# Optimization experiments

Hardware: AMD Instinct MI355X
Metric: run time of the kernel (lower is better)

The kernel has to match this reference:

```python
import jax, jax.numpy as jnp
import numpy as np

TAU_MEM, TAU_SYN = 20.0, 5.0
THRESHOLD, BETA, RESET = 1.0, 4.0, 0.0
ALPHA_MEM = float(np.exp(-1.0 / TAU_MEM))
ALPHA_SYN = float(np.exp(-1.0 / TAU_SYN))
EPS = 1e-6


def _lif(x, W, b):
    # x: [B,T,D] -> spikes_with_grad: [B,T,H] (faithful to original incl. the
    # spikes + stop_grad(spikes - surrogate) expression, forward value 2*s - sg)
    cur = jnp.einsum('btd,dh->bth', x, W) + b  # all-timestep projection (same math as per-step dense)
    B, T, H = cur.shape
    v0 = jnp.zeros((B, H), cur.dtype)
    i0 = jnp.zeros((B, H), cur.dtype)

    def step(carry, ic):
        v, i = carry
        i = ALPHA_SYN * i + ic
        v = ALPHA_MEM * v + (1.0 - ALPHA_MEM) * i
        spikes = (v >= THRESHOLD).astype(jnp.float32)
        sg = BETA / (2.0 * (1.0 + jnp.cosh(BETA * (v - THRESHOLD))))
        swg = spikes + jax.lax.stop_gradient(spikes - sg)
        v = jnp.where(spikes > 0, RESET, v)
        return (v, i), swg

    (_, _), out = jax.lax.scan(step, (v0, i0), cur.transpose(1, 0, 2))
    return out.transpose(1, 0, 2)


def _layernorm(x, scale, bias):
    mu = jnp.mean(x, axis=-1, keepdims=True)
    var = jnp.var(x, axis=-1, keepdims=True)
    return (x - mu) * jax.lax.rsqrt(var + EPS) * scale + bias


def setup_inputs() -> dict:
    key = jax.random.key(0)
    ks = jax.random.split(key, 8)
    B, T, D = 512, 128, 512
    H0, H1, H2, C = 256, 128, 64, 2
    s = 0.02
    return {
        'spike_trains': jax.random.uniform(ks[0], (B, T, D), jnp.float32),
        'W0': jax.random.normal(ks[1], (D, H0), jnp.float32) * s,
        'b0': jnp.zeros((H0,), jnp.float32),
        'ln1_scale': jnp.ones((H0,), jnp.float32),
        'ln1_bias': jnp.zeros((H0,), jnp.float32),
        'W1': jax.random.normal(ks[2], (H0, H1), jnp.float32) * s,
        'b1': jnp.zeros((H1,), jnp.float32),
        'ln2_scale': jnp.ones((H1,), jnp.float32),
        'ln2_bias': jnp.zeros((H1,), jnp.float32),
        'W2': jax.random.normal(ks[3], (H1, H2), jnp.float32) * s,
        'b2': jnp.zeros((H2,), jnp.float32),
        'Wc': jax.random.normal(ks[4], (H2, C), jnp.float32) * s,
        'bc': jnp.zeros((C,), jnp.float32),
    }


def reference(spike_trains, W0, b0, ln1_scale, ln1_bias, W1, b1,
              ln2_scale, ln2_bias, W2, b2, Wc, bc):
    x = _lif(spike_trains, W0, b0)                    # layer 0: no pre-norm
    x = _lif(_layernorm(x, ln1_scale, ln1_bias), W1, b1)
    x = _lif(_layernorm(x, ln2_scale, ln2_bias), W2, b2)
    pooled = jnp.mean(x, axis=1)                      # [B, H2]
    logits = pooled @ Wc + bc                         # [B, C]
    return logits, pooled, jnp.mean(x)
```

## Files before the change

kernel.cpp:

```cpp
#include <hip/hip_runtime.h>
#include <cstddef>

static constexpr float A_MEM  = 0.951229424500714f;
static constexpr float A_SYN  = 0.8187307530779818f;
static constexpr float OM_MEM = 0.04877057549928599f;

__global__ __launch_bounds__(256) void gemm_bias(
    const float* __restrict__ A, const float* __restrict__ W,
    const float* __restrict__ bias, float* __restrict__ C,
    int M, int K, int N)
{
    __shared__ float As[16][64];
    __shared__ float Ws[16][64];
    const int tid = threadIdx.x;
    const int tx = tid & 15;
    const int ty = tid >> 4;
    const int mBase = blockIdx.y * 64;
    const int nBase = blockIdx.x * 64;

    const int arow = tid >> 2;
    const int acol = (tid & 3) << 2;
    const int wrow = tid >> 4;
    const int wcol = (tid & 15) << 2;

    float acc[4][4] = {};
    for (int k0 = 0; k0 < K; k0 += 16) {
        float4 av = *(const float4*)(A + (size_t)(mBase + arow) * K + (k0 + acol));
        float4 wv = *(const float4*)(W + (size_t)(k0 + wrow) * N + (nBase + wcol));
        __syncthreads();
        As[acol + 0][arow] = av.x;
        As[acol + 1][arow] = av.y;
        As[acol + 2][arow] = av.z;
        As[acol + 3][arow] = av.w;
        *(float4*)&Ws[wrow][wcol] = wv;
        __syncthreads();
        #pragma unroll
        for (int kk = 0; kk < 16; ++kk) {
            float4 a = *(const float4*)&As[kk][ty << 2];
            float4 b = *(const float4*)&Ws[kk][tx << 2];
            float ar[4] = {a.x, a.y, a.z, a.w};
            float br[4] = {b.x, b.y, b.z, b.w};
            #pragma unroll
            for (int i2 = 0; i2 < 4; ++i2)
                #pragma unroll
                for (int j = 0; j < 4; ++j)
                    acc[i2][j] += ar[i2] * br[j];
        }
    }
    const int cn = nBase + (tx << 2);
    float4 bv = *(const float4*)(bias + cn);
    float bb[4] = {bv.x, bv.y, bv.z, bv.w};
    #pragma unroll
    for (int i2 = 0; i2 < 4; ++i2) {
        const int cm = mBase + (ty << 2) + i2;
        float4 o;
        o.x = acc[i2][0] + bb[0];
        o.y = acc[i2][1] + bb[1];
        o.z = acc[i2][2] + bb[2];
        o.w = acc[i2][3] + bb[3];
        *(float4*)(C + (size_t)cm * N + cn) = o;
    }
}

template<bool POOL>
__global__ __launch_bounds__(256) void lif_scan(
    const float* __restrict__ cur, float* __restrict__ out,
    float* __restrict__ pooled, int T, int H)
{
    const int idx = blockIdx.x * 256 + threadIdx.x;
    const int b = idx / H;
    const int h = idx - b * H;
    const float* cp = cur + (size_t)b * T * H + h;
    float* op = out ? out + (size_t)b * T * H + h : nullptr;
    float v = 0.f, cin = 0.f, sum = 0.f;
    for (int t = 0; t < T; ++t) {
        float ic = cp[(size_t)t * H];
        cin = A_SYN * cin + ic;
        v = A_MEM * v + OM_MEM * cin;
        float s = (v >= 1.0f) ? 1.0f : 0.0f;
        float xx = 4.0f * (v - 1.0f);
        float ch2 = __expf(xx) + __expf(-xx);
        float sg = 4.0f / (2.0f + ch2);
        float o = 2.0f * s - sg;
        if (POOL) sum += o;
        else op[(size_t)t * H] = o;
        if (s > 0.f) v = 0.0f;
    }
    if (POOL) pooled[idx] = sum * (1.0f / 128.0f);
}

template<int H>
__global__ __launch_bounds__(256) void layernorm_k(
    const float* __restrict__ x, const float* __restrict__ scale,
    const float* __restrict__ bias, float* __restrict__ y)
{
    constexpr int VPL = H / 64;
    const int wave = threadIdx.x >> 6;
    const int lane = threadIdx.x & 63;
    const size_t row = (size_t)blockIdx.x * 4 + wave;
    const float* xp = x + row * H + lane * VPL;
    float vals[VPL];
    #pragma unroll
    for (int j = 0; j < VPL; ++j) vals[j] = xp[j];
    float s = 0.f, ss = 0.f;
    #pragma unroll
    for (int j = 0; j < VPL; ++j) { s += vals[j]; ss += vals[j] * vals[j]; }
    #pragma unroll
    for (int off = 32; off; off >>= 1) {
        s  += __shfl_xor(s, off);
        ss += __shfl_xor(ss, off);
    }
    const float mu  = s * (1.0f / H);
    const float var = ss * (1.0f / H) - mu * mu;
    const float rs  = rsqrtf(var + 1e-6f);
    float* yp = y + row * H + lane * VPL;
    #pragma unroll
    for (int j = 0; j < VPL; ++j)
        yp[j] = (vals[j] - mu) * rs * scale[lane * VPL + j] + bias[lane * VPL + j];
}

__global__ __launch_bounds__(1024) void head_k(
    const float* __restrict__ pooled, const float* __restrict__ Wc,
    const float* __restrict__ bc, float* __restrict__ logits,
    float* __restrict__ meanp)
{
    const int tid = threadIdx.x;
    const int b = tid >> 1, c = tid & 1;
    float accl = 0.f;
    #pragma unroll 8
    for (int k = 0; k < 64; ++k) accl += pooled[b * 64 + k] * Wc[k * 2 + c];
    logits[tid] = accl + bc[c];

    float s = 0.f;
    for (int i2 = tid; i2 < 512 * 64; i2 += 1024) s += pooled[i2];
    #pragma unroll
    for (int off = 32; off; off >>= 1) s += __shfl_xor(s, off);
    __shared__ float red[16];
    const int wave = tid >> 6, lane = tid & 63;
    if (lane == 0) red[wave] = s;
    __syncthreads();
    if (tid == 0) {
        float tot = 0.f;
        #pragma unroll
        for (int w = 0; w < 16; ++w) tot += red[w];
        meanp[0] = tot * (1.0f / 32768.0f);
    }
}

extern "C" void kernel_launch(void* const* d_in, const int* in_sizes, int n_in,
                              void* d_out, int out_size, void* d_ws, size_t ws_size,
                              hipStream_t stream) {
    const float* x    = (const float*)d_in[0];
    const float* W0   = (const float*)d_in[1];
    const float* b0   = (const float*)d_in[2];
    const float* ln1s = (const float*)d_in[3];
    const float* ln1b = (const float*)d_in[4];
    const float* W1   = (const float*)d_in[5];
    const float* b1   = (const float*)d_in[6];
    const float* ln2s = (const float*)d_in[7];
    const float* ln2b = (const float*)d_in[8];
    const float* W2   = (const float*)d_in[9];
    const float* b2   = (const float*)d_in[10];
    const float* Wc   = (const float*)d_in[11];
    const float* bc   = (const float*)d_in[12];

    float* out    = (float*)d_out;
    float* logits = out;
    float* pooled = out + 1024;
    float* meanp  = out + 1024 + 32768;

    const int B = 512, T = 128, M = B * T;
    float* bufA = (float*)d_ws;
    float* bufB = bufA + (size_t)M * 256;

    gemm_bias<<<dim3(256 / 64, M / 64), 256, 0, stream>>>(x, W0, b0, bufA, M, 512, 256);
    lif_scan<false><<<(B * 256) / 256, 256, 0, stream>>>(bufA, bufB, nullptr, T, 256);
    layernorm_k<256><<<M / 4, 256, 0, stream>>>(bufB, ln1s, ln1b, bufA);
    gemm_bias<<<dim3(128 / 64, M / 64), 256, 0, stream>>>(bufA, W1, b1, bufB, M, 256, 128);
    lif_scan<false><<<(B * 128) / 256, 256, 0, stream>>>(bufB, bufA, nullptr, T, 128);
    layernorm_k<128><<<M / 4, 256, 0, stream>>>(bufA, ln2s, ln2b, bufB);
    gemm_bias<<<dim3(64 / 64, M / 64), 256, 0, stream>>>(bufB, W2, b2, bufA, M, 128, 64);
    lif_scan<true><<<(B * 64) / 256, 256, 0, stream>>>(bufA, nullptr, pooled, T, 64);
    head_k<<<1, 1024, 0, stream>>>(pooled, Wc, bc, logits, meanp);
}
```

Before: 657.9 us.

## Fuse GEMM, LIF scan and layernorm into one per-batch kernel per layer

Each layer becomes a single kernel with one block per batch element. The block computes the full [128 x H] projection tile in registers, stages it in LDS, runs the LIF scan over time from shared memory, then applies layernorm and writes the next layer's input. This removes the global round-trips of the intermediate currents and spikes and cuts the launch count. The cost is large dynamic shared memory (up to 128 KB), which allows only one block per CU, plus a serial scan that uses only H threads while the others sit idle.

```diff
diff --git a/kernel.cpp b/kernel.cpp
--- a/kernel.cpp
+++ b/kernel.cpp
@@ -5,118 +5,161 @@
 static constexpr float A_SYN  = 0.8187307530779818f;
 static constexpr float OM_MEM = 0.04877057549928599f;
 
-__global__ __launch_bounds__(256) void gemm_bias(
+template<int NT, int K, int H, bool LN, bool POOL>
+__global__ __launch_bounds__(NT) void layer_fused(
     const float* __restrict__ A, const float* __restrict__ W,
-    const float* __restrict__ bias, float* __restrict__ C,
-    int M, int K, int N)
+    const float* __restrict__ bias,
+    const float* __restrict__ lns, const float* __restrict__ lnb,
+    float* __restrict__ out)
 {
-    __shared__ float As[16][64];
-    __shared__ float Ws[16][64];
-    const int tid = threadIdx.x;
-    const int tx = tid & 15;
-    const int ty = tid >> 4;
-    const int mBase = blockIdx.y * 64;
-    const int nBase = blockIdx.x * 64;
-
-    const int arow = tid >> 2;
-    const int acol = (tid & 3) << 2;
-    const int wrow = tid >> 4;
-    const int wcol = (tid & 15) << 2;
-
-    float acc[4][4] = {};
-    for (int k0 = 0; k0 < K; k0 += 16) {
-        float4 av = *(const float4*)(A + (size_t)(mBase + arow) * K + (k0 + acol));
-        float4 wv = *(const float4*)(W + (size_t)(k0 + wrow) * N + (nBase + wcol));
-        __syncthreads();
-        As[acol + 0][arow] = av.x;
-        As[acol + 1][arow] = av.y;
-        As[acol + 2][arow] = av.z;
-        As[acol + 3][arow] = av.w;
-        *(float4*)&Ws[wrow][wcol] = wv;
-        __syncthreads();
+  constexpr int T = 128;
+  constexpr int BK = 16;
+  constexpr int TXB = (NT == 512) ? 5 : 4;
+  constexpr int NTX = 1 << TXB;
+  constexpr int NJ  = H / NTX;
+  constexpr int S   = K / BK;
+  constexpr int APT = (BK * 128 / 4) / NT;
+  constexpr int WPT = (BK * H / 4) / NT < 1 ? 1 : (BK * H / 4) / NT;
+  extern __shared__ __align__(16) float smem[];
+  float* As  = smem;
+  float* Ws  = smem + BK * 128;
+  float* buf = smem;
+
+  const int b   = blockIdx.x;
+  const int tid = threadIdx.x;
+  const int tx  = tid & (NTX - 1);
+  const int ty  = tid >> TXB;
+  const float* Ab = A + (size_t)b * T * K;
+
+  float acc[8][NJ];
+  #pragma unroll
+  for (int i = 0; i < 8; ++i)
+    #pragma unroll
+    for (int j = 0; j < NJ; ++j) acc[i][j] = 0.f;
+
+  float4 aR[APT], wR[WPT];
+  auto load_tile = [&](int k0) {
+    #pragma unroll
+    for (int p = 0; p < APT; ++p) {
+      int f4 = tid + p * NT;
+      int r  = f4 >> 2;
+      int c4 = (f4 & 3) << 2;
+      aR[p] = *(const float4*)(Ab + (size_t)r * K + k0 + c4);
+    }
+    #pragma unroll
+    for (int p = 0; p < WPT; ++p) {
+      int f4 = tid + p * NT;
+      int k  = f4 / (H / 4);
+      int c4 = (f4 % (H / 4)) << 2;
+      wR[p] = *(const float4*)(W + (size_t)(k0 + k) * H + c4);
+    }
+  };
+
+  load_tile(0);
+  for (int s = 0; s < S; ++s) {
+    __syncthreads();
+    #pragma unroll
+    for (int p = 0; p < APT; ++p) {
+      int f4 = tid + p * NT;
+      int r  = f4 >> 2;
+      int c4 = (f4 & 3) << 2;
+      As[(c4 + 0) * 128 + r] = aR[p].x;
+      As[(c4 + 1) * 128 + r] = aR[p].y;
+      As[(c4 + 2) * 128 + r] = aR[p].z;
+      As[(c4 + 3) * 128 + r] = aR[p].w;
+    }
+    #pragma unroll
+    for (int p = 0; p < WPT; ++p) {
+      int f4 = tid + p * NT;
+      int k  = f4 / (H / 4);
+      int c4 = (f4 % (H / 4)) << 2;
+      *(float4*)(Ws + k * H + c4) = wR[p];
+    }
+    __syncthreads();
+    if (s + 1 < S) load_tile((s + 1) * BK);
+    #pragma unroll
+    for (int kk = 0; kk < BK; ++kk) {
+      float4 a0 = *(const float4*)(As + kk * 128 + ty * 8);
+      float4 a1 = *(const float4*)(As + kk * 128 + ty * 8 + 4);
+      float av[8] = {a0.x, a0.y, a0.z, a0.w, a1.x, a1.y, a1.z, a1.w};
+      float bv[NJ];
+      #pragma unroll
+      for (int j = 0; j < NJ; ++j) bv[j] = Ws[kk * H + j * NTX + tx];
+      #pragma unroll
+      for (int i = 0; i < 8; ++i)
         #pragma unroll
-        for (int kk = 0; kk < 16; ++kk) {
-            float4 a = *(const float4*)&As[kk][ty << 2];
-            float4 b = *(const float4*)&Ws[kk][tx << 2];
-            float ar[4] = {a.x, a.y, a.z, a.w};
-            float br[4] = {b.x, b.y, b.z, b.w};
-            #pragma unroll
-            for (int i2 = 0; i2 < 4; ++i2)
-                #pragma unroll
-                for (int j = 0; j < 4; ++j)
-                    acc[i2][j] += ar[i2] * br[j];
-        }
-    }
-    const int cn = nBase + (tx << 2);
-    float4 bv = *(const float4*)(bias + cn);
-    float bb[4] = {bv.x, bv.y, bv.z, bv.w};
-    #pragma unroll
-    for (int i2 = 0; i2 < 4; ++i2) {
-        const int cm = mBase + (ty << 2) + i2;
-        float4 o;
-        o.x = acc[i2][0] + bb[0];
-        o.y = acc[i2][1] + bb[1];
-        o.z = acc[i2][2] + bb[2];
-        o.w = acc[i2][3] + bb[3];
-        *(float4*)(C + (size_t)cm * N + cn) = o;
-    }
-}
-
-template<bool POOL>
-__global__ __launch_bounds__(256) void lif_scan(
-    const float* __restrict__ cur, float* __restrict__ out,
-    float* __restrict__ pooled, int T, int H)
-{
-    const int idx = blockIdx.x * 256 + threadIdx.x;
-    const int b = idx / H;
-    const int h = idx - b * H;
-    const float* cp = cur + (size_t)b * T * H + h;
-    float* op = out ? out + (size_t)b * T * H + h : nullptr;
+        for (int j = 0; j < NJ; ++j)
+          acc[i][j] += av[i] * bv[j];
+    }
+  }
+
+  __syncthreads();
+  {
+    float bb[NJ];
+    #pragma unroll
+    for (int j = 0; j < NJ; ++j) bb[j] = bias[j * NTX + tx];
+    #pragma unroll
+    for (int i = 0; i < 8; ++i) {
+      int row = ty * 8 + i;
+      #pragma unroll
+      for (int j = 0; j < NJ; ++j)
+        buf[row * H + j * NTX + tx] = acc[i][j] + bb[j];
+    }
+  }
+  __syncthreads();
+
+  if (tid < H) {
     float v = 0.f, cin = 0.f, sum = 0.f;
     for (int t = 0; t < T; ++t) {
-        float ic = cp[(size_t)t * H];
-        cin = A_SYN * cin + ic;
-        v = A_MEM * v + OM_MEM * cin;
-        float s = (v >= 1.0f) ? 1.0f : 0.0f;
-        float xx = 4.0f * (v - 1.0f);
-        float ch2 = __expf(xx) + __expf(-xx);
-        float sg = 4.0f / (2.0f + ch2);
-        float o = 2.0f * s - sg;
-        if (POOL) sum += o;
-        else op[(size_t)t * H] = o;
-        if (s > 0.f) v = 0.0f;
-    }
-    if (POOL) pooled[idx] = sum * (1.0f / 128.0f);
-}
-
-template<int H>
-__global__ __launch_bounds__(256) void layernorm_k(
-    const float* __restrict__ x, const float* __restrict__ scale,
-    const float* __restrict__ bias, float* __restrict__ y)
-{
+      float ic = buf[t * H + tid];
+      cin = A_SYN * cin + ic;
+      v = A_MEM * v + OM_MEM * cin;
+      bool sp = (v >= 1.0f);
+      float xx = 4.0f * (v - 1.0f);
+      float e  = __expf(xx);
+      float tp = 1.0f + e;
+      float sg = 4.0f * e / (tp * tp);
+      float o  = (sp ? 2.0f : 0.0f) - sg;
+      if (POOL) sum += o;
+      else buf[t * H + tid] = o;
+      v = sp ? 0.0f : v;
+    }
+    if (POOL) out[(size_t)b * H + tid] = sum * (1.0f / 128.0f);
+  }
+
+  if (LN) {
+    __syncthreads();
     constexpr int VPL = H / 64;
-    const int wave = threadIdx.x >> 6;
-    const int lane = threadIdx.x & 63;
-    const size_t row = (size_t)blockIdx.x * 4 + wave;
-    const float* xp = x + row * H + lane * VPL;
-    float vals[VPL];
-    #pragma unroll
-    for (int j = 0; j < VPL; ++j) vals[j] = xp[j];
-    float s = 0.f, ss = 0.f;
-    #pragma unroll
-    for (int j = 0; j < VPL; ++j) { s += vals[j]; ss += vals[j] * vals[j]; }
-    #pragma unroll
-    for (int off = 32; off; off >>= 1) {
-        s  += __shfl_xor(s, off);
-        ss += __shfl_xor(ss, off);
-    }
-    const float mu  = s * (1.0f / H);
-    const float var = ss * (1.0f / H) - mu * mu;
-    const float rs  = rsqrtf(var + 1e-6f);
-    float* yp = y + row * H + lane * VPL;
-    #pragma unroll
-    for (int j = 0; j < VPL; ++j)
-        yp[j] = (vals[j] - mu) * rs * scale[lane * VPL + j] + bias[lane * VPL + j];
+    constexpr int NW  = NT / 64;
+    const int wv   = tid >> 6;
+    const int lane = tid & 63;
+    float sc[VPL], bi[VPL];
+    #pragma unroll
+    for (int q = 0; q < VPL; ++q) {
+      sc[q] = lns[lane * VPL + q];
+      bi[q] = lnb[lane * VPL + q];
+    }
+    for (int t = wv; t < T; t += NW) {
+      float vals[VPL];
+      #pragma unroll
+      for (int q = 0; q < VPL; ++q) vals[q] = buf[t * H + lane * VPL + q];
+      float s1 = 0.f, s2 = 0.f;
+      #pragma unroll
+      for (int q = 0; q < VPL; ++q) { s1 += vals[q]; s2 += vals[q] * vals[q]; }
+      #pragma unroll
+      for (int off = 32; off; off >>= 1) {
+        s1 += __shfl_xor(s1, off);
+        s2 += __shfl_xor(s2, off);
+      }
+      float mu  = s1 * (1.0f / H);
+      float var = s2 * (1.0f / H) - mu * mu;
+      float rs  = rsqrtf(var + 1e-6f);
+      float* op = out + ((size_t)b * T + t) * H + lane * VPL;
+      #pragma unroll
+      for (int q = 0; q < VPL; ++q)
+        op[q] = (vals[q] - mu) * rs * sc[q] + bi[q];
+    }
+  }
 }
 
 __global__ __launch_bounds__(1024) void head_k(
@@ -169,17 +212,22 @@
     float* pooled = out + 1024;
     float* meanp  = out + 1024 + 32768;
 
-    const int B = 512, T = 128, M = B * T;
-    float* bufA = (float*)d_ws;
-    float* bufB = bufA + (size_t)M * 256;
-
-    gemm_bias<<<dim3(256 / 64, M / 64), 256, 0, stream>>>(x, W0, b0, bufA, M, 512, 256);
-    lif_scan<false><<<(B * 256) / 256, 256, 0, stream>>>(bufA, bufB, nullptr, T, 256);
-    layernorm_k<256><<<M / 4, 256, 0, stream>>>(bufB, ln1s, ln1b, bufA);
-    gemm_bias<<<dim3(128 / 64, M / 64), 256, 0, stream>>>(bufA, W1, b1, bufB, M, 256, 128);
-    lif_scan<false><<<(B * 128) / 256, 256, 0, stream>>>(bufB, bufA, nullptr, T, 128);
-    layernorm_k<128><<<M / 4, 256, 0, stream>>>(bufA, ln2s, ln2b, bufB);
-    gemm_bias<<<dim3(64 / 64, M / 64), 256, 0, stream>>>(bufB, W2, b2, bufA, M, 128, 64);
-    lif_scan<true><<<(B * 64) / 256, 256, 0, stream>>>(bufA, nullptr, pooled, T, 64);
+    const int B = 512;
+    float* y1 = (float*)d_ws;
+    float* y2 = y1 + (size_t)65536 * 256;
+
+    (void)hipFuncSetAttribute((const void*)&layer_fused<512,512,256,true,false>,
+                              hipFuncAttributeMaxDynamicSharedMemorySize, 131072);
+    (void)hipFuncSetAttribute((const void*)&layer_fused<256,256,128,true,false>,
+                              hipFuncAttributeMaxDynamicSharedMemorySize, 65536);
+    (void)hipFuncSetAttribute((const void*)&layer_fused<256,128,64,false,true>,
+                              hipFuncAttributeMaxDynamicSharedMemorySize, 32768);
+
+    layer_fused<512,512,256,true,false><<<B, 512, 131072, stream>>>(
+        x,  W0, b0, ln1s, ln1b, y1);
+    layer_fused<256,256,128,true,false><<<B, 256, 65536, stream>>>(
+        y1, W1, b1, ln2s, ln2b, y2);
+    layer_fused<256,128,64,false,true><<<B, 256, 32768, stream>>>(
+        y2, W2, b2, nullptr, nullptr, pooled);
     head_k<<<1, 1024, 0, stream>>>(pooled, Wc, bc, logits, meanp);
 }
```

Result: faster. 639.5 us (-2.8%).
